# Optimization experiments

Measured on AMD Instinct MI355X. Metric: run time of the kernel, lower is better.

The kernel has to match this reference:

```python
import jax, jax.numpy as jnp
import numpy as np

NUM_LAYERS = 2
DIM_Z = 128
NORM = float(np.sqrt(DIM_Z))
EPS = 1e-5


def _ln(v):
    # LayerNorm(elementwise_affine=False) over last dim
    m = v.mean(-1, keepdims=True)
    var = ((v - m) ** 2).mean(-1, keepdims=True)
    return (v - m) / jnp.sqrt(var + EPS)


def setup_inputs() -> dict:
    key = jax.random.key(0)
    ks = jax.random.split(key, 8)
    B, C, P = 32, 128, 128
    K, DS = 510, 256
    H = W = 64
    return {
        "x": jax.random.normal(ks[0], (B, C, P), jnp.float32),
        "latents": jax.random.normal(ks[1], (K, DS), jnp.float32),
        "blank_latent": jax.random.normal(ks[2], (NUM_LAYERS, DIM_Z), jnp.float32),
        "linear_w": jax.random.normal(ks[3], (DIM_Z, DS), jnp.float32) * 0.05,
        "linear_b": jnp.zeros((DIM_Z,), jnp.float32),
        "anchors_w": jax.random.normal(ks[4], (DIM_Z, C), jnp.float32) * 0.05,
        "anchors_b": jnp.zeros((DIM_Z,), jnp.float32),
        "prototypes": jax.random.uniform(ks[5], (K, 3, H, W), dtype=jnp.float32),
        "masks": jax.random.uniform(ks[6], (K, 1, H, W), dtype=jnp.float32),
    }


def reference(x, latents, blank_latent, linear_w, linear_b, anchors_w, anchors_b, prototypes, masks):
    B, C, P = x.shape
    L = NUM_LAYERS
    # codebook latents: (K, dim_sprites) -> Linear -> LN -> (K, dim_z)
    lat = _ln(latents @ linear_w.T + linear_b)
    xp = jnp.transpose(x, (0, 2, 1))                          # (B, P, C)
    a = _ln(xp.reshape(B * P, C) @ anchors_w.T + anchors_b)   # (B*P, dim_z)
    logits_main = a @ lat.T                                   # (B*P, K)
    # blank logits: position p uses blank_latent[p % L]; value repeated L times
    blank_pp = blank_latent[jnp.arange(P) % L]                # (P, dim_z == C)
    dots = jnp.einsum('bpc,pc->bp', xp, blank_pp)             # (B, P)
    logits_blank = jnp.broadcast_to(dots.reshape(B * P, 1), (B * P, L))
    logits = jnp.concatenate([logits_main, logits_blank], axis=-1) / NORM
    weights = jax.nn.softmax(logits, axis=-1)                 # (B*P, K+L)
    log_probs = jax.nn.log_softmax(
        jnp.transpose(logits.reshape(B, P, -1), (1, 0, 2)), axis=2)  # (P, B, K+L)
    # sprite bank: [prototypes;0] on rgb, [masks;0] on alpha -> (K+L, 4, H, W)
    zp = jnp.zeros((L,) + prototypes.shape[1:], prototypes.dtype)
    zm = jnp.zeros((L,) + masks.shape[1:], masks.dtype)
    sprite = jnp.concatenate(
        [jnp.concatenate([prototypes, zp], axis=0),
         jnp.concatenate([masks, zm], axis=0)], axis=1)
    # broadcast-multiply-reduce expressed as a single contraction
    S = jnp.einsum('nk,kchw->nchw', weights, sprite)          # (B*P, 4, H, W)
    H_, W_ = S.shape[-2], S.shape[-1]
    S_out = jnp.transpose(S.reshape(B, P, 4, H_, W_), (1, 0, 2, 3, 4))  # (P, B, 4, H, W)
    return (weights, logits, log_probs, S_out)
```

## Files before the change

### kernel.cpp

```cpp
#include <hip/hip_runtime.h>

typedef unsigned short u16;
typedef unsigned int u32;
typedef __bf16 bf16x8 __attribute__((ext_vector_type(8)));
typedef float f32x4 __attribute__((ext_vector_type(4)));

#define EPS 1e-5f
#define INV_NORM 0.088388347648318447f

#define OUT_W   0
#define OUT_LOG 2097152
#define OUT_LP  4194304
#define OUT_S   6291456

#define WS_BT   0
#define WS_LAT  8388608
#define WS_A    8454144

__device__ __forceinline__ u16 f2b(float f) {
  u32 i = __float_as_uint(f);
  return (u16)((i + 0x7FFFu + ((i >> 16) & 1u)) >> 16);
}
__device__ __forceinline__ float wsum(float v) {
#pragma unroll
  for (int off = 32; off > 0; off >>= 1) v += __shfl_down(v, off, 64);
  return v;
}
__device__ __forceinline__ float wmax(float v) {
#pragma unroll
  for (int off = 32; off > 0; off >>= 1) v = fmaxf(v, __shfl_down(v, off, 64));
  return v;
}
__device__ __forceinline__ float dot8(uint4 u, const float* xp) {
  float s;
  s  = xp[0] * __uint_as_float(u.x << 16);
  s += xp[1] * __uint_as_float(u.x & 0xFFFF0000u);
  s += xp[2] * __uint_as_float(u.y << 16);
  s += xp[3] * __uint_as_float(u.y & 0xFFFF0000u);
  s += xp[4] * __uint_as_float(u.z << 16);
  s += xp[5] * __uint_as_float(u.z & 0xFFFF0000u);
  s += xp[6] * __uint_as_float(u.w << 16);
  s += xp[7] * __uint_as_float(u.w & 0xFFFF0000u);
  return s;
}
__device__ __forceinline__ float dot4(float4 u, const float* xp) {
  return xp[0] * u.x + xp[1] * u.y + xp[2] * u.z + xp[3] * u.w;
}

__global__ __launch_bounds__(128) void k_lat(const float* __restrict__ latents,
                                             const float* __restrict__ lw,
                                             const float* __restrict__ lb,
                                             u16* __restrict__ latbf) {
  int k = blockIdx.x, t = threadIdx.x;
  int wid = t >> 6, lane = t & 63;
  __shared__ float ls[256];
  __shared__ float red[4];
  ls[t] = latents[k * 256 + t];
  ls[t + 128] = latents[k * 256 + 128 + t];
  __syncthreads();
  float v = lb[t];
  const float4* wv = (const float4*)(lw + t * 256);
#pragma unroll
  for (int c = 0; c < 64; c++) v += dot4(wv[c], &ls[c * 4]);
  float s = wsum(v), s2 = wsum(v * v);
  if (lane == 0) { red[wid * 2] = s; red[wid * 2 + 1] = s2; }
  __syncthreads();
  float mean = (red[0] + red[2]) * 0.0078125f;
  float var = (red[1] + red[3]) * 0.0078125f - mean * mean;
  latbf[k * 128 + t] = f2b((v - mean) * rsqrtf(var + EPS));
}

__global__ __launch_bounds__(256) void k_tr(const float* __restrict__ proto,
                                            const float* __restrict__ masks,
                                            u16* __restrict__ Bt) {
  __shared__ u16 tile[64 * 72];
  int t = threadIdx.x;
  int n0 = blockIdx.x * 64;
  int k0 = blockIdx.y * 64;
  int ch = n0 >> 12, hw0 = n0 & 4095;
  int r = t >> 2, c = (t & 3) * 16;
  int kg = k0 + r;
  u16 vals[16];
#pragma unroll
  for (int e = 0; e < 16; e++) vals[e] = 0;
  if (kg < 510) {
    const float* src = (ch < 3) ? (proto + ((size_t)kg * 3 + ch) * 4096 + hw0 + c)
                                : (masks + (size_t)kg * 4096 + hw0 + c);
    const float4* s4 = (const float4*)src;
#pragma unroll
    for (int q = 0; q < 4; q++) {
      float4 u = s4[q];
      vals[q * 4 + 0] = f2b(u.x);
      vals[q * 4 + 1] = f2b(u.y);
      vals[q * 4 + 2] = f2b(u.z);
      vals[q * 4 + 3] = f2b(u.w);
    }
  }
#pragma unroll
  for (int e = 0; e < 16; e++) tile[r * 72 + c + e] = vals[e];
  __syncthreads();
  int nr = t >> 2, kc = (t & 3) * 16;
  u32 u[8];
#pragma unroll
  for (int e = 0; e < 8; e++) {
    u32 lo = tile[(kc + 2 * e) * 72 + nr];
    u32 hi = tile[(kc + 2 * e + 1) * 72 + nr];
    u[e] = lo | (hi << 16);
  }
  u16* dst = Bt + (size_t)(n0 + nr) * 512 + k0 + kc;
  uint4 v0 = {u[0], u[1], u[2], u[3]};
  uint4 v1 = {u[4], u[5], u[6], u[7]};
  *(uint4*)dst = v0;
  *(uint4*)(dst + 8) = v1;
}

__global__ __launch_bounds__(128) void k_rows(const float* __restrict__ x,
                                              const float* __restrict__ aw,
                                              const float* __restrict__ ab,
                                              const float* __restrict__ blank,
                                              const u16* __restrict__ latbf,
                                              float* __restrict__ out,
                                              u16* __restrict__ Abf) {
  int n = blockIdx.x;
  int b = n >> 7, p = n & 127;
  int t = threadIdx.x, wid = t >> 6, lane = t & 63;
  __shared__ float xs[128];
  __shared__ float ash[128];
  __shared__ float red[8];
  xs[t] = x[(size_t)b * 16384 + (size_t)t * 128 + p];
  __syncthreads();
  float av = ab[t];
  const float4* awv = (const float4*)(aw + t * 128);
#pragma unroll
  for (int c = 0; c < 32; c++) av += dot4(awv[c], &xs[c * 4]);
  float bv = xs[t] * blank[(p & 1) * 128 + t];
  float s = wsum(av), s2 = wsum(av * av), sb = wsum(bv);
  if (lane == 0) { red[wid * 3] = s; red[wid * 3 + 1] = s2; red[wid * 3 + 2] = sb; }
  __syncthreads();
  float mean = (red[0] + red[3]) * 0.0078125f;
  float var = (red[1] + red[4]) * 0.0078125f - mean * mean;
  float dots = red[2] + red[5];
  float an = (av - mean) * rsqrtf(var + EPS);
  ash[t] = an;
  float bl = dots * INV_NORM;
  __syncthreads();
  float l[4];
  float lmax = -1e30f;
#pragma unroll
  for (int i = 0; i < 4; i++) {
    int k = i * 128 + t;
    float v;
    if (k < 510) {
      const uint4* lv = (const uint4*)(latbf + k * 128);
      float acc = 0.f;
#pragma unroll
      for (int c = 0; c < 16; c++) acc += dot8(lv[c], &ash[c * 8]);
      v = acc * INV_NORM;
    } else {
      v = bl;
    }
    l[i] = v;
    lmax = fmaxf(lmax, v);
  }
  float m = wmax(lmax);
  __syncthreads();
  if (lane == 0) red[wid] = m;
  __syncthreads();
  float M = fmaxf(red[0], red[1]);
  float se = 0.f;
#pragma unroll
  for (int i = 0; i < 4; i++) se += expf(l[i] - M);
  float ssum = wsum(se);
  __syncthreads();
  if (lane == 0) red[wid] = ssum;
  __syncthreads();
  float S = red[0] + red[1];
  float logZ = M + logf(S);
  size_t nb = (size_t)n * 512;
  size_t lpb = (size_t)OUT_LP + ((size_t)p * 32 + b) * 512;
#pragma unroll
  for (int i = 0; i < 4; i++) {
    int k = i * 128 + t;
    float lp = l[i] - logZ;
    float w = expf(lp);
    out[OUT_W + nb + k] = w;
    out[OUT_LOG + nb + k] = l[i];
    out[lpb + k] = lp;
    Abf[nb + k] = f2b(w);
  }
}

__global__ __launch_bounds__(256) void k_gemm(const u16* __restrict__ A,
                                              const u16* __restrict__ Bt,
                                              float* __restrict__ out) {
  __shared__ u16 As[128 * 32];
  __shared__ u16 Bs[128 * 32];
  int tid = threadIdx.x;
  int wid = tid >> 6, lane = tid & 63;
  int nBase = blockIdx.x * 128;
  int mBase = blockIdx.y * 128;
  int wm = wid >> 1, wn = wid & 1;
  int quad = lane >> 4, r16 = lane & 15;
  f32x4 acc[4][4];
#pragma unroll
  for (int i = 0; i < 4; i++)
#pragma unroll
    for (int j = 0; j < 4; j++) acc[i][j] = (f32x4){0.f, 0.f, 0.f, 0.f};

  int srow = wid * 32 + (lane >> 2);
  int koff = (lane & 3) * 8;
  char* ldsA = (char*)As + wid * 2048;
  char* ldsB = (char*)Bs + wid * 2048;

  for (int kt = 0; kt < 16; kt++) {
    int k0 = kt * 32;
#pragma unroll
    for (int c = 0; c < 2; c++) {
      const u16* ga = A + (size_t)(mBase + srow + c * 16) * 512 + k0 + koff;
      const u16* gb = Bt + (size_t)(nBase + srow + c * 16) * 512 + k0 + koff;
      __builtin_amdgcn_global_load_lds(
          (__attribute__((address_space(1))) void*)ga,
          (__attribute__((address_space(3))) void*)(ldsA + c * 1024), 16, 0, 0);
      __builtin_amdgcn_global_load_lds(
          (__attribute__((address_space(1))) void*)gb,
          (__attribute__((address_space(3))) void*)(ldsB + c * 1024), 16, 0, 0);
    }
    __syncthreads();
    bf16x8 af[4], bfr[4];
#pragma unroll
    for (int i = 0; i < 4; i++)
      af[i] = *(const bf16x8*)&As[(wm * 64 + i * 16 + r16) * 32 + quad * 8];
#pragma unroll
    for (int j = 0; j < 4; j++)
      bfr[j] = *(const bf16x8*)&Bs[(wn * 64 + j * 16 + r16) * 32 + quad * 8];
#pragma unroll
    for (int i = 0; i < 4; i++)
#pragma unroll
      for (int j = 0; j < 4; j++)
        acc[i][j] = __builtin_amdgcn_mfma_f32_16x16x32_bf16(af[i], bfr[j],
                                                            acc[i][j], 0, 0, 0);
    __syncthreads();
  }
#pragma unroll
  for (int i = 0; i < 4; i++) {
#pragma unroll
    for (int r = 0; r < 4; r++) {
      int mg = mBase + wm * 64 + i * 16 + quad * 4 + r;
      size_t orow = (size_t)((mg & 127) * 32 + (mg >> 7));
      float* orp = out + OUT_S + orow * 16384 + nBase + wn * 64 + r16;
#pragma unroll
      for (int j = 0; j < 4; j++) orp[j * 16] = acc[i][j][r];
    }
  }
}

extern "C" void kernel_launch(void* const* d_in, const int* in_sizes, int n_in,
                              void* d_out, int out_size, void* d_ws, size_t ws_size,
                              hipStream_t stream) {
  const float* x = (const float*)d_in[0];
  const float* latents = (const float*)d_in[1];
  const float* blank = (const float*)d_in[2];
  const float* lw = (const float*)d_in[3];
  const float* lb = (const float*)d_in[4];
  const float* aw = (const float*)d_in[5];
  const float* ab = (const float*)d_in[6];
  const float* proto = (const float*)d_in[7];
  const float* masks = (const float*)d_in[8];
  float* out = (float*)d_out;
  u16* ws16 = (u16*)d_ws;
  u16* Bt = ws16 + WS_BT;
  u16* latbf = ws16 + WS_LAT;
  u16* Abf = ws16 + WS_A;

  k_lat<<<510, 128, 0, stream>>>(latents, lw, lb, latbf);
  k_tr<<<dim3(256, 8), 256, 0, stream>>>(proto, masks, Bt);
  k_rows<<<4096, 128, 0, stream>>>(x, aw, ab, blank, latbf, out, Abf);
  k_gemm<<<dim3(128, 32), 256, 0, stream>>>(Abf, Bt, out);
}
```

Before: 533.8 us.

## Widen GEMM K-tile with swizzled LDS and vectorize softmax logit stores

The sprite GEMM now stages 64-wide K tiles (8 iterations instead of 16) and applies an XOR swizzle to the LDS layout to avoid bank conflicts on the MFMA fragment reads. This halves the number of barriers per K sweep but doubles the LDS footprint. The softmax kernel now gives each thread four consecutive codebook entries instead of a 128-stride pattern, so the weights, logits, log-probs and bf16 weight stores can be written as float4 and uint2 vectors. The latent reads change from coalesced across threads to per-thread contiguous rows, which may hurt access efficiency for those loads.

```diff
diff --git a/kernel.cpp b/kernel.cpp
--- a/kernel.cpp
+++ b/kernel.cpp
@@ -144,24 +144,22 @@
   ash[t] = an;
   float bl = dots * INV_NORM;
   __syncthreads();
+  const uint4* lv = (const uint4*)(latbf + (size_t)(4 * t) * 128);
+  float a0 = 0.f, a1 = 0.f, a2 = 0.f, a3 = 0.f;
+#pragma unroll
+  for (int c = 0; c < 16; c++) {
+    const float* ap = &ash[c * 8];
+    a0 += dot8(lv[c], ap);
+    a1 += dot8(lv[16 + c], ap);
+    a2 += dot8(lv[32 + c], ap);
+    a3 += dot8(lv[48 + c], ap);
+  }
   float l[4];
-  float lmax = -1e30f;
-#pragma unroll
-  for (int i = 0; i < 4; i++) {
-    int k = i * 128 + t;
-    float v;
-    if (k < 510) {
-      const uint4* lv = (const uint4*)(latbf + k * 128);
-      float acc = 0.f;
-#pragma unroll
-      for (int c = 0; c < 16; c++) acc += dot8(lv[c], &ash[c * 8]);
-      v = acc * INV_NORM;
-    } else {
-      v = bl;
-    }
-    l[i] = v;
-    lmax = fmaxf(lmax, v);
-  }
+  l[0] = a0 * INV_NORM;
+  l[1] = a1 * INV_NORM;
+  l[2] = (4 * t + 2 < 510) ? a2 * INV_NORM : bl;
+  l[3] = (4 * t + 3 < 510) ? a3 * INV_NORM : bl;
+  float lmax = fmaxf(fmaxf(l[0], l[1]), fmaxf(l[2], l[3]));
   float m = wmax(lmax);
   __syncthreads();
   if (lane == 0) red[wid] = m;
@@ -176,25 +174,33 @@
   __syncthreads();
   float S = red[0] + red[1];
   float logZ = M + logf(S);
-  size_t nb = (size_t)n * 512;
-  size_t lpb = (size_t)OUT_LP + ((size_t)p * 32 + b) * 512;
+  size_t nb = (size_t)n * 512 + 4 * t;
+  size_t lpb = (size_t)OUT_LP + ((size_t)p * 32 + b) * 512 + 4 * t;
+  float4 wv4, lg4, lp4;
+  u16 ab4[4];
+  float* lpv = &lp4.x;
+  float* wvv = &wv4.x;
+  float* lgv = &lg4.x;
 #pragma unroll
   for (int i = 0; i < 4; i++) {
-    int k = i * 128 + t;
     float lp = l[i] - logZ;
     float w = expf(lp);
-    out[OUT_W + nb + k] = w;
-    out[OUT_LOG + nb + k] = l[i];
-    out[lpb + k] = lp;
-    Abf[nb + k] = f2b(w);
-  }
+    lpv[i] = lp;
+    wvv[i] = w;
+    lgv[i] = l[i];
+    ab4[i] = f2b(w);
+  }
+  *(float4*)(out + OUT_W + nb) = wv4;
+  *(float4*)(out + OUT_LOG + nb) = lg4;
+  *(float4*)(out + lpb) = lp4;
+  *(uint2*)(Abf + nb) = *(uint2*)ab4;
 }
 
 __global__ __launch_bounds__(256) void k_gemm(const u16* __restrict__ A,
                                               const u16* __restrict__ Bt,
                                               float* __restrict__ out) {
-  __shared__ u16 As[128 * 32];
-  __shared__ u16 Bs[128 * 32];
+  __shared__ u16 As[128 * 64];
+  __shared__ u16 Bs[128 * 64];
   int tid = threadIdx.x;
   int wid = tid >> 6, lane = tid & 63;
   int nBase = blockIdx.x * 128;
@@ -207,38 +213,44 @@
 #pragma unroll
     for (int j = 0; j < 4; j++) acc[i][j] = (f32x4){0.f, 0.f, 0.f, 0.f};
 
-  int srow = wid * 32 + (lane >> 2);
-  int koff = (lane & 3) * 8;
-  char* ldsA = (char*)As + wid * 2048;
-  char* ldsB = (char*)Bs + wid * 2048;
-
-  for (int kt = 0; kt < 16; kt++) {
-    int k0 = kt * 32;
-#pragma unroll
-    for (int c = 0; c < 2; c++) {
-      const u16* ga = A + (size_t)(mBase + srow + c * 16) * 512 + k0 + koff;
-      const u16* gb = Bt + (size_t)(nBase + srow + c * 16) * 512 + k0 + koff;
+  int srow8 = wid * 8 + (lane >> 3);
+  int kx = ((lane & 7) ^ (lane >> 3)) * 8;
+  char* ldsA = (char*)As + wid * 1024;
+  char* ldsB = (char*)Bs + wid * 1024;
+  int sw = r16 & 7;
+
+  for (int kt = 0; kt < 8; kt++) {
+    int k0 = kt * 64;
+#pragma unroll
+    for (int q = 0; q < 4; q++) {
+      int row = q * 32 + srow8;
+      const u16* ga = A + (size_t)(mBase + row) * 512 + k0 + kx;
+      const u16* gb = Bt + (size_t)(nBase + row) * 512 + k0 + kx;
       __builtin_amdgcn_global_load_lds(
           (__attribute__((address_space(1))) void*)ga,
-          (__attribute__((address_space(3))) void*)(ldsA + c * 1024), 16, 0, 0);
+          (__attribute__((address_space(3))) void*)(ldsA + q * 4096), 16, 0, 0);
       __builtin_amdgcn_global_load_lds(
           (__attribute__((address_space(1))) void*)gb,
-          (__attribute__((address_space(3))) void*)(ldsB + c * 1024), 16, 0, 0);
+          (__attribute__((address_space(3))) void*)(ldsB + q * 4096), 16, 0, 0);
     }
     __syncthreads();
-    bf16x8 af[4], bfr[4];
-#pragma unroll
-    for (int i = 0; i < 4; i++)
-      af[i] = *(const bf16x8*)&As[(wm * 64 + i * 16 + r16) * 32 + quad * 8];
-#pragma unroll
-    for (int j = 0; j < 4; j++)
-      bfr[j] = *(const bf16x8*)&Bs[(wn * 64 + j * 16 + r16) * 32 + quad * 8];
-#pragma unroll
-    for (int i = 0; i < 4; i++)
+#pragma unroll
+    for (int kk = 0; kk < 2; kk++) {
+      int ch = ((quad + 4 * kk) ^ sw) * 8;
+      bf16x8 af[4], bfr[4];
+#pragma unroll
+      for (int i = 0; i < 4; i++)
+        af[i] = *(const bf16x8*)&As[(wm * 64 + i * 16 + r16) * 64 + ch];
 #pragma unroll
       for (int j = 0; j < 4; j++)
-        acc[i][j] = __builtin_amdgcn_mfma_f32_16x16x32_bf16(af[i], bfr[j],
-                                                            acc[i][j], 0, 0, 0);
+        bfr[j] = *(const bf16x8*)&Bs[(wn * 64 + j * 16 + r16) * 64 + ch];
+#pragma unroll
+      for (int i = 0; i < 4; i++)
+#pragma unroll
+        for (int j = 0; j < 4; j++)
+          acc[i][j] = __builtin_amdgcn_mfma_f32_16x16x32_bf16(af[i], bfr[j],
+                                                              acc[i][j], 0, 0, 0);
+    }
     __syncthreads();
   }
 #pragma unroll
```

Result: faster. 514.9 us (-3.5%).
